# Kernel tuning notes

Measured on AMD Instinct MI355X. Metric: run time of the kernel, lower is better.

The kernel has to match this reference:

```python
import jax, jax.numpy as jnp
import numpy as np

BETA = 0.5  # hard-negative concentration (module default)


def _l2norm(x, axis):
    return x / jnp.linalg.norm(x, axis=axis, keepdims=True)


def setup_inputs() -> dict:
    key = jax.random.key(0)
    k1, k2, k3 = jax.random.split(key, 3)
    B, V, D = 4096, 2, 512
    features = jax.random.normal(k1, (B, V, D), dtype=jnp.float32)
    out_1 = jax.random.normal(k2, (B, D), dtype=jnp.float32)
    out_2 = jax.random.normal(k3, (B, D), dtype=jnp.float32)
    indexes = jnp.arange(B, dtype=jnp.int64)
    return {"features": features, "out_1": out_1, "out_2": out_2, "indexes": indexes}


def reference(features, out_1, out_2, indexes):
    # features is normalized in the original forward but unused afterwards
    _ = _l2norm(features, axis=2)

    o1 = _l2norm(out_1, axis=-1)
    o2 = _l2norm(out_2, axis=-1)
    out = jnp.concatenate([o1, o2], axis=0)            # [2B, D]
    label = jnp.concatenate([indexes, indexes], axis=0)  # [2B]
    batch = label.shape[0]

    # cost = exp(2 * out @ out.T), [2B, 2B]
    cost = jnp.exp(2.0 * jnp.einsum('id,jd->ij', out, out))

    pos_full = (label[:, None] == label[None, :]).astype(cost.dtype)
    neg_index = 1.0 - pos_full
    pos_index = pos_full - jnp.eye(batch, dtype=cost.dtype)

    pos = pos_index * cost
    neg = neg_index * cost

    # importance weights: neg_index * exp(beta * log(neg)) == neg_index * neg**beta
    imp = jax.lax.stop_gradient(neg_index * jnp.power(neg, BETA))
    neg_exp_sum = (imp * neg).sum(axis=-1) / imp.sum(axis=-1)  # [2B]

    denom = pos + (batch - 2) * neg_exp_sum[:, None]
    ratio = pos / denom

    mask = pos_index > 0
    safe_ratio = jnp.where(mask, ratio, 1.0)
    nce = -(jnp.log(safe_ratio) * pos_index).sum() / pos_index.sum()
    return nce
```

## Files before the change

### kernel.cpp

```cpp
#include <hip/hip_runtime.h>
#include <stdint.h>

#define BHALF 4096
#define NROWS 8192
#define DDIM  512
#define KNEG  8190.0f

#define BM   128
#define BK   32
#define NTIL 64
#define TBLK (NTIL * (NTIL + 1) / 2)
#define FABLK 256

typedef short v8s __attribute__((ext_vector_type(8)));
typedef float v4f __attribute__((ext_vector_type(4)));

static __device__ inline float bf2f(uint32_t u) {
    union { uint32_t i; float f; } c; c.i = u << 16; return c.f;
}
static __device__ inline uint32_t f2bf(float f) {
    union { float f; uint32_t i; } c; c.f = f;
    return (c.i + 0x7fffu + ((c.i >> 16) & 1u)) >> 16;
}

#define GLL16(gp, lp)                                                         \
    __builtin_amdgcn_global_load_lds(                                         \
        (__attribute__((address_space(1))) void*)(gp),                        \
        (__attribute__((address_space(3))) void*)(lp), 16, 0, 0)

__global__ __launch_bounds__(256) void rownorm_cvt_kernel(
    const void* __restrict__ o1, const void* __restrict__ o2,
    float* __restrict__ rn, uint16_t* __restrict__ cvt)
{
    int wave = threadIdx.x >> 6, lane = threadIdx.x & 63;
    int row = blockIdx.x * 4 + wave;

    uint32_t w = ((const uint32_t*)o1)[lane * 977 + 13];
    uint32_t e = (w >> 7) & 0xFFu;
    int bad = (e < 100u || e > 140u) ? 1 : 0;
    #pragma unroll
    for (int m = 32; m; m >>= 1) bad += __shfl_xor(bad, m);

    float ss;
    uint4 pack;
    if (bad <= 16) {
        const uint16_t* s = (row < BHALF)
            ? (const uint16_t*)o1 + (size_t)row * DDIM
            : (const uint16_t*)o2 + (size_t)(row - BHALF) * DDIM;
        pack = ((const uint4*)s)[lane];
        float a0 = bf2f(pack.x & 0xffffu), a1 = bf2f(pack.x >> 16);
        float a2 = bf2f(pack.y & 0xffffu), a3 = bf2f(pack.y >> 16);
        float a4 = bf2f(pack.z & 0xffffu), a5 = bf2f(pack.z >> 16);
        float a6 = bf2f(pack.w & 0xffffu), a7 = bf2f(pack.w >> 16);
        ss = a0*a0 + a1*a1 + a2*a2 + a3*a3 + a4*a4 + a5*a5 + a6*a6 + a7*a7;
    } else {
        const float* s = (row < BHALF)
            ? (const float*)o1 + (size_t)row * DDIM
            : (const float*)o2 + (size_t)(row - BHALF) * DDIM;
        float4 a = ((const float4*)s)[2 * lane];
        float4 b = ((const float4*)s)[2 * lane + 1];
        ss = a.x*a.x + a.y*a.y + a.z*a.z + a.w*a.w
           + b.x*b.x + b.y*b.y + b.z*b.z + b.w*b.w;
        pack.x = f2bf(a.x) | (f2bf(a.y) << 16);
        pack.y = f2bf(a.z) | (f2bf(a.w) << 16);
        pack.z = f2bf(b.x) | (f2bf(b.y) << 16);
        pack.w = f2bf(b.z) | (f2bf(b.w) << 16);
    }
    *(uint4*)(cvt + (size_t)row * DDIM + lane * 8) = pack;

    #pragma unroll
    for (int m = 32; m; m >>= 1) ss += __shfl_xor(ss, m);
    if (lane == 0) rn[row] = rsqrtf(ss);
}

__global__ __launch_bounds__(256, 3) void SupCon_hcl_49323404427556_kernel(
    const uint16_t* __restrict__ cvt, const float* __restrict__ rn,
    float* __restrict__ pden, float* __restrict__ pnum, float* __restrict__ cpos)
{
    __shared__ alignas(16) uint16_t la[BM * BK];
    __shared__ alignas(16) uint16_t lb[BM * BK];
    __shared__ float rnA[BM], rnB[BM];
    __shared__ float s_dr[BM][2], s_nr[BM][2], s_dc[BM][2], s_nc[BM][2];

    int tid  = threadIdx.x;
    int wave = tid >> 6, lane = tid & 63;
    int quad = lane >> 4, l16 = lane & 15;
    int wrow = (wave >> 1) * 64, wcol = (wave & 1) * 64;

    int t = blockIdx.x;
    int bi = (int)(64.5f - sqrtf(64.5f * 64.5f - 2.0f * (float)t));
    while (bi > 0 && (64 * bi - (bi * (bi - 1)) / 2) > t) --bi;
    while ((64 * (bi + 1) - ((bi + 1) * bi) / 2) <= t) ++bi;
    int bj = bi + (t - (64 * bi - (bi * (bi - 1)) / 2));
    int i0 = bi * BM, j0 = bj * BM;
    bool diag = (bi == bj);
    bool partner = (bj == bi + 32) && (bi < 32);
    bool plain = !diag && !partner;

    if (tid < BM) rnA[tid] = rn[i0 + tid];
    else          rnB[tid - BM] = rn[j0 + (tid - BM)];

    const uint16_t* A16 = cvt + (size_t)i0 * DDIM;
    const uint16_t* B16 = cvt + (size_t)j0 * DDIM;

    v4f acc[4][4];
    v4f z = {0.f, 0.f, 0.f, 0.f};
    #pragma unroll
    for (int a = 0; a < 4; ++a)
        #pragma unroll
        for (int b = 0; b < 4; ++b) acc[a][b] = z;

    int rloc = lane >> 2;
    int slot = lane & 3;
    int rA   = 32 * wave + rloc;
    int chk  = (slot - (rA >> 1)) & 3;
    const uint16_t* gA = A16 + (size_t)rA * DDIM + chk * 8;
    const uint16_t* gB = B16 + (size_t)rA * DDIM + chk * 8;
    uint16_t* sA0 = &la[(32 * wave) * BK];
    uint16_t* sA1 = &la[(32 * wave + 16) * BK];
    uint16_t* sB0 = &lb[(32 * wave) * BK];
    uint16_t* sB1 = &lb[(32 * wave + 16) * BK];

    const uint16_t* lbp = diag ? la : lb;
    int sfrag = (quad + (l16 >> 1)) & 3;

    for (int kb = 0; kb < DDIM / BK; ++kb) {
        __syncthreads();
        GLL16(gA + kb * BK, sA0);
        GLL16(gA + kb * BK + 16 * DDIM, sA1);
        if (!diag) {
            GLL16(gB + kb * BK, sB0);
            GLL16(gB + kb * BK + 16 * DDIM, sB1);
        }
        __syncthreads();

        v8s af[4], bfr[4];
        #pragma unroll
        for (int tt = 0; tt < 4; ++tt) {
            af[tt]  = *(const v8s*)(&la [(wrow + 16 * tt + l16) * BK + sfrag * 8]);
            bfr[tt] = *(const v8s*)(&lbp[(wcol + 16 * tt + l16) * BK + sfrag * 8]);
        }
        #pragma unroll
        for (int mt = 0; mt < 4; ++mt)
            #pragma unroll
            for (int nt = 0; nt < 4; ++nt)
                acc[mt][nt] = __builtin_amdgcn_mfma_f32_16x16x32_bf16(
                    af[mt], bfr[nt], acc[mt][nt], 0, 0, 0);
    }

    if (plain) {
        float rjv[4];
        #pragma unroll
        for (int nt = 0; nt < 4; ++nt) rjv[nt] = rnB[wcol + 16 * nt + l16];

        float pd[16], pn[16], cdv[4], cnv[4];
        #pragma unroll
        for (int k = 0; k < 16; ++k) { pd[k] = 0.f; pn[k] = 0.f; }
        #pragma unroll
        for (int nt = 0; nt < 4; ++nt) { cdv[nt] = 0.f; cnv[nt] = 0.f; }

        #pragma unroll
        for (int mt = 0; mt < 4; ++mt) {
            #pragma unroll
            for (int r = 0; r < 4; ++r) {
                float ri = rnA[wrow + 16 * mt + quad * 4 + r];
                #pragma unroll
                for (int nt = 0; nt < 4; ++nt) {
                    float e  = __expf(acc[mt][nt][r] * ri * rjv[nt]);
                    float e3 = e * e * e;
                    pd[mt * 4 + r] += e;   pn[mt * 4 + r] += e3;
                    cdv[nt]        += e;   cnv[nt]        += e3;
                }
            }
        }

        #define BSTEP(arr, n, bit)                                            \
            _Pragma("unroll")                                                 \
            for (int p = 0; p < (n); ++p) {                                   \
                float mine = (l16 & (bit)) ? arr[2*p+1] : arr[2*p];           \
                float send = (l16 & (bit)) ? arr[2*p]   : arr[2*p+1];         \
                arr[p] = mine + __shfl_xor(send, (bit));                      \
            }
        BSTEP(pd, 8, 1) BSTEP(pd, 4, 2) BSTEP(pd, 2, 4) BSTEP(pd, 1, 8)
        BSTEP(pn, 8, 1) BSTEP(pn, 4, 2) BSTEP(pn, 2, 4) BSTEP(pn, 1, 8)
        #undef BSTEP

        int rowk = wrow + 16 * (l16 >> 2) + quad * 4 + (l16 & 3);
        s_dr[rowk][wcol >> 6] = pd[0];
        s_nr[rowk][wcol >> 6] = pn[0];

        #pragma unroll
        for (int nt = 0; nt < 4; ++nt) {
            float cd = cdv[nt] + __shfl_xor(cdv[nt], 16);
            cd += __shfl_xor(cd, 32);
            float cn = cnv[nt] + __shfl_xor(cnv[nt], 16);
            cn += __shfl_xor(cn, 32);
            if (quad == 0) {
                s_dc[wcol + 16 * nt + l16][wrow >> 6] = cd;
                s_nc[wcol + 16 * nt + l16][wrow >> 6] = cn;
            }
        }
    } else {
        #pragma unroll
        for (int mt = 0; mt < 4; ++mt) {
            #pragma unroll
            for (int nt = 0; nt < 4; ++nt) {
                float rj = rnB[wcol + 16 * nt + l16];
                #pragma unroll
                for (int r = 0; r < 4; ++r) {
                    float ri = rnA[wrow + 16 * mt + quad * 4 + r];
                    acc[mt][nt][r] = __expf(acc[mt][nt][r] * ri * rj);
                }
            }
        }

        #pragma unroll
        for (int mt = 0; mt < 4; ++mt) {
            #pragma unroll
            for (int r = 0; r < 4; ++r) {
                int gil = wrow + 16 * mt + quad * 4 + r;
                int gi = i0 + gil;
                int pr = gi ^ BHALF;
                float pdv = 0.f, pnv = 0.f;
                #pragma unroll
                for (int nt = 0; nt < 4; ++nt) {
                    int gj = j0 + wcol + 16 * nt + l16;
                    float e = acc[mt][nt][r];
                    if (gj == pr) cpos[gi] = e * e;
                    if (gj != gi && gj != pr) { pdv += e; pnv += e * e * e; }
                }
                #pragma unroll
                for (int m = 1; m < 16; m <<= 1) {
                    pdv += __shfl_xor(pdv, m);
                    pnv += __shfl_xor(pnv, m);
                }
                if (l16 == 0) { s_dr[gil][wcol >> 6] = pdv; s_nr[gil][wcol >> 6] = pnv; }
            }
        }

        if (!diag) {
            #pragma unroll
            for (int nt = 0; nt < 4; ++nt) {
                int gjl = wcol + 16 * nt + l16;
                int gj = j0 + gjl;
                int pj = gj ^ BHALF;
                float cd = 0.f, cn = 0.f;
                #pragma unroll
                for (int mt = 0; mt < 4; ++mt) {
                    #pragma unroll
                    for (int r = 0; r < 4; ++r) {
                        int gi = i0 + wrow + 16 * mt + quad * 4 + r;
                        float e = acc[mt][nt][r];
                        if (gi == pj) cpos[gj] = e * e;
                        else { cd += e; cn += e * e * e; }
                    }
                }
                cd += __shfl_xor(cd, 16); cn += __shfl_xor(cn, 16);
                cd += __shfl_xor(cd, 32); cn += __shfl_xor(cn, 32);
                if (quad == 0) { s_dc[gjl][wrow >> 6] = cd; s_nc[gjl][wrow >> 6] = cn; }
            }
        }
    }

    __syncthreads();
    if (tid < BM) {
        pden[(size_t)bj * NROWS + i0 + tid] = s_dr[tid][0] + s_dr[tid][1];
        pnum[(size_t)bj * NROWS + i0 + tid] = s_nr[tid][0] + s_nr[tid][1];
        if (!diag) {
            pden[(size_t)bi * NROWS + j0 + tid] = s_dc[tid][0] + s_dc[tid][1];
            pnum[(size_t)bi * NROWS + j0 + tid] = s_nc[tid][0] + s_nc[tid][1];
        }
    }
}

__global__ __launch_bounds__(256) void finalizeA_kernel(
    const float* __restrict__ pden, const float* __restrict__ pnum,
    const float* __restrict__ cpos, float* __restrict__ bpart)
{
    int b = blockIdx.x, t = threadIdx.x;
    int r = b * 32 + (t & 31);
    int c = t >> 5;
    float pd = 0.f, pn = 0.f;
    #pragma unroll
    for (int i = 0; i < 8; ++i) {
        int x = c + 8 * i;
        pd += pden[(size_t)x * NROWS + r];
        pn += pnum[(size_t)x * NROWS + r];
    }
    pd += __shfl_xor(pd, 32);
    pn += __shfl_xor(pn, 32);

    __shared__ float sd[4][32], sn[4][32];
    int wave = t >> 6, lane = t & 63;
    if (lane < 32) { sd[wave][lane] = pd; sn[wave][lane] = pn; }
    __syncthreads();

    float s = 0.f;
    if (t < 32) {
        float d = sd[0][t] + sd[1][t] + sd[2][t] + sd[3][t];
        float n = sn[0][t] + sn[1][t] + sn[2][t] + sn[3][t];
        s = logf(1.0f + KNEG * (n / d) / cpos[b * 32 + t]);
    }
    if (t < 64) {
        #pragma unroll
        for (int m = 32; m; m >>= 1) s += __shfl_xor(s, m);
        if (t == 0) bpart[b] = s;
    }
}

__global__ __launch_bounds__(256) void finalizeB_kernel(
    const float* __restrict__ bpart, float* __restrict__ out)
{
    int t = threadIdx.x;
    float s = bpart[t];
    #pragma unroll
    for (int m = 32; m; m >>= 1) s += __shfl_xor(s, m);
    __shared__ float wsum[4];
    if ((t & 63) == 0) wsum[t >> 6] = s;
    __syncthreads();
    if (t == 0) out[0] = (wsum[0] + wsum[1] + wsum[2] + wsum[3]) / (float)NROWS;
}

extern "C" void kernel_launch(void* const* d_in, const int* in_sizes, int n_in,
                              void* d_out, int out_size, void* d_ws, size_t ws_size,
                              hipStream_t stream)
{
    const void* o1 = d_in[1];
    const void* o2 = d_in[2];

    uint16_t* cvt = (uint16_t*)d_ws;
    float* pden = (float*)(cvt + (size_t)NROWS * DDIM);
    float* pnum = pden + (size_t)NTIL * NROWS;
    float* rn   = pnum + (size_t)NTIL * NROWS;
    float* cpos = rn + NROWS;
    float* bpart= cpos + NROWS;

    rownorm_cvt_kernel<<<NROWS / 4, 256, 0, stream>>>(o1, o2, rn, cvt);
    SupCon_hcl_49323404427556_kernel<<<TBLK, 256, 0, stream>>>(cvt, rn, pden, pnum, cpos);
    finalizeA_kernel<<<FABLK, 256, 0, stream>>>(pden, pnum, cpos, bpart);
    finalizeB_kernel<<<1, 256, 0, stream>>>(bpart, (float*)d_out);
}
```

Before: 135.3 us.

## Pre-swizzle bf16 rows into MFMA fragment layout and load fragments directly from global

The conversion kernel now writes the bf16 copy of the normalized inputs in a tiled layout whose 16-byte chunks match the 16x16x32 MFMA operand fragments. The GEMM kernel then reads each wave's A and B fragments straight from global memory with contiguous per-lane loads. This removes the LDS staging buffers and the two barriers per K step. Block indices are also remapped so consecutive triangle tiles are spread across the 8 XCDs. The cost is that operand reuse between waves now relies on the L1/L2 caches instead of shared memory, with no explicit prefetch to hide global load latency.

New measurement: 135.8 us. No clear change (+0.3%).

```diff
diff --git a/kernel.cpp b/kernel.cpp
--- a/kernel.cpp
+++ b/kernel.cpp
@@ -23,14 +23,10 @@
     return (c.i + 0x7fffu + ((c.i >> 16) & 1u)) >> 16;
 }
 
-#define GLL16(gp, lp)                                                         \
-    __builtin_amdgcn_global_load_lds(                                         \
-        (__attribute__((address_space(1))) void*)(gp),                        \
-        (__attribute__((address_space(3))) void*)(lp), 16, 0, 0)
 
 __global__ __launch_bounds__(256) void rownorm_cvt_kernel(
     const void* __restrict__ o1, const void* __restrict__ o2,
-    float* __restrict__ rn, uint16_t* __restrict__ cvt)
+    float* __restrict__ rn, uint16_t* __restrict__ cvt2)
 {
     int wave = threadIdx.x >> 6, lane = threadIdx.x & 63;
     int row = blockIdx.x * 4 + wave;
@@ -66,7 +62,9 @@
         pack.z = f2bf(b.x) | (f2bf(b.y) << 16);
         pack.w = f2bf(b.z) | (f2bf(b.w) << 16);
     }
-    *(uint4*)(cvt + (size_t)row * DDIM + lane * 8) = pack;
+    size_t byteoff = (size_t)(row >> 4) * 16384 + (size_t)lane * 256
+                   + (size_t)(row & 15) * 16;
+    *(uint4*)((char*)cvt2 + byteoff) = pack;
 
     #pragma unroll
     for (int m = 32; m; m >>= 1) ss += __shfl_xor(ss, m);
@@ -74,11 +72,9 @@
 }
 
 __global__ __launch_bounds__(256, 3) void SupCon_hcl_49323404427556_kernel(
-    const uint16_t* __restrict__ cvt, const float* __restrict__ rn,
+    const uint16_t* __restrict__ cvt2, const float* __restrict__ rn,
     float* __restrict__ pden, float* __restrict__ pnum, float* __restrict__ cpos)
 {
-    __shared__ alignas(16) uint16_t la[BM * BK];
-    __shared__ alignas(16) uint16_t lb[BM * BK];
     __shared__ float rnA[BM], rnB[BM];
     __shared__ float s_dr[BM][2], s_nr[BM][2], s_dc[BM][2], s_nc[BM][2];
 
@@ -87,7 +83,9 @@
     int quad = lane >> 4, l16 = lane & 15;
     int wrow = (wave >> 1) * 64, wcol = (wave & 1) * 64;
 
-    int t = blockIdx.x;
+    int b = blockIdx.x;
+    int t = (b & 7) * (TBLK / 8) + (b >> 3);
+
     int bi = (int)(64.5f - sqrtf(64.5f * 64.5f - 2.0f * (float)t));
     while (bi > 0 && (64 * bi - (bi * (bi - 1)) / 2) > t) --bi;
     while ((64 * (bi + 1) - ((bi + 1) * bi) / 2) <= t) ++bi;
@@ -99,46 +97,26 @@
 
     if (tid < BM) rnA[tid] = rn[i0 + tid];
     else          rnB[tid - BM] = rn[j0 + (tid - BM)];
-
-    const uint16_t* A16 = cvt + (size_t)i0 * DDIM;
-    const uint16_t* B16 = cvt + (size_t)j0 * DDIM;
+    __syncthreads();
+
+    const char* cb = (const char*)cvt2;
+    const char* a0 = cb + (size_t)((i0 + wrow) >> 4) * 16384 + (size_t)lane * 16;
+    const char* b0 = cb + (size_t)((j0 + wcol) >> 4) * 16384 + (size_t)lane * 16;
 
     v4f acc[4][4];
     v4f z = {0.f, 0.f, 0.f, 0.f};
     #pragma unroll
     for (int a = 0; a < 4; ++a)
         #pragma unroll
-        for (int b = 0; b < 4; ++b) acc[a][b] = z;
-
-    int rloc = lane >> 2;
-    int slot = lane & 3;
-    int rA   = 32 * wave + rloc;
-    int chk  = (slot - (rA >> 1)) & 3;
-    const uint16_t* gA = A16 + (size_t)rA * DDIM + chk * 8;
-    const uint16_t* gB = B16 + (size_t)rA * DDIM + chk * 8;
-    uint16_t* sA0 = &la[(32 * wave) * BK];
-    uint16_t* sA1 = &la[(32 * wave + 16) * BK];
-    uint16_t* sB0 = &lb[(32 * wave) * BK];
-    uint16_t* sB1 = &lb[(32 * wave + 16) * BK];
-
-    const uint16_t* lbp = diag ? la : lb;
-    int sfrag = (quad + (l16 >> 1)) & 3;
-
+        for (int bb = 0; bb < 4; ++bb) acc[a][bb] = z;
+
+    #pragma unroll 2
     for (int kb = 0; kb < DDIM / BK; ++kb) {
-        __syncthreads();
-        GLL16(gA + kb * BK, sA0);
-        GLL16(gA + kb * BK + 16 * DDIM, sA1);
-        if (!diag) {
-            GLL16(gB + kb * BK, sB0);
-            GLL16(gB + kb * BK + 16 * DDIM, sB1);
-        }
-        __syncthreads();
-
         v8s af[4], bfr[4];
         #pragma unroll
         for (int tt = 0; tt < 4; ++tt) {
-            af[tt]  = *(const v8s*)(&la [(wrow + 16 * tt + l16) * BK + sfrag * 8]);
-            bfr[tt] = *(const v8s*)(&lbp[(wcol + 16 * tt + l16) * BK + sfrag * 8]);
+            af[tt]  = *(const v8s*)(a0 + (size_t)tt * 16384 + (size_t)kb * 1024);
+            bfr[tt] = *(const v8s*)(b0 + (size_t)tt * 16384 + (size_t)kb * 1024);
         }
         #pragma unroll
         for (int mt = 0; mt < 4; ++mt)
@@ -328,15 +306,15 @@
     const void* o1 = d_in[1];
     const void* o2 = d_in[2];
 
-    uint16_t* cvt = (uint16_t*)d_ws;
-    float* pden = (float*)(cvt + (size_t)NROWS * DDIM);
+    uint16_t* cvt2 = (uint16_t*)d_ws;
+    float* pden = (float*)(cvt2 + (size_t)NROWS * DDIM);
     float* pnum = pden + (size_t)NTIL * NROWS;
     float* rn   = pnum + (size_t)NTIL * NROWS;
     float* cpos = rn + NROWS;
     float* bpart= cpos + NROWS;
 
-    rownorm_cvt_kernel<<<NROWS / 4, 256, 0, stream>>>(o1, o2, rn, cvt);
-    SupCon_hcl_49323404427556_kernel<<<TBLK, 256, 0, stream>>>(cvt, rn, pden, pnum, cpos);
+    rownorm_cvt_kernel<<<NROWS / 4, 256, 0, stream>>>(o1, o2, rn, cvt2);
+    SupCon_hcl_49323404427556_kernel<<<TBLK, 256, 0, stream>>>(cvt2, rn, pden, pnum, cpos);
     finalizeA_kernel<<<FABLK, 256, 0, stream>>>(pden, pnum, cpos, bpart);
     finalizeB_kernel<<<1, 256, 0, stream>>>(bpart, (float*)d_out);
 }
```
